# Performance work log

Hardware: AMD Instinct MI355X
Metric: run time of the kernel (lower is better)

Reference implementation:

```python
import jax, jax.numpy as jnp
import numpy as np

B, T, D, H = 2, 2048, 768, 12
HS = D // H           # head_size = 64
FF = 4 * D            # feed_forward_multiplier = 4 -> hidden 3072
HALF = FF // 2        # SwiGLU halves hidden -> 1536
EPS = 1e-8


def rmsnorm(x, scale):
    # RMSNorm with p=-1: full-dim L2 norm / sqrt(d), then x/(rms+eps)*scale
    d = x.shape[-1]
    rms = jnp.linalg.norm(x, axis=-1, keepdims=True) * (d ** -0.5)
    return scale * (x / (rms + EPS))


def setup_inputs() -> dict:
    key = jax.random.key(0)
    ks = jax.random.split(key, 12)
    s = 0.02
    return {
        "x":  jax.random.normal(ks[0], (B, T, D), dtype=jnp.float32),
        "Wq": jax.random.normal(ks[1], (H, D, HS), dtype=jnp.float32) * s,
        "Wk": jax.random.normal(ks[2], (H, D, HS), dtype=jnp.float32) * s,
        "Wv": jax.random.normal(ks[3], (H, D, HS), dtype=jnp.float32) * s,
        "Wo": jax.random.normal(ks[4], (D, D), dtype=jnp.float32) * s,
        "bo": jnp.zeros((D,), dtype=jnp.float32),
        "W1": jax.random.normal(ks[5], (D, FF), dtype=jnp.float32) * s,
        "b1": jnp.zeros((FF,), dtype=jnp.float32),
        "W2": jax.random.normal(ks[6], (HALF, D), dtype=jnp.float32) * s,
        "b2": jnp.zeros((D,), dtype=jnp.float32),
        "g1": jnp.ones((D,), dtype=jnp.float32),
        "g2": jnp.ones((D,), dtype=jnp.float32),
    }


def reference(x, Wq, Wk, Wv, Wo, bo, W1, b1, W2, b2, g1, g2):
    Bx, Tx, Dx = x.shape
    # --- Multi-head causal attention (pre-RMSNorm, residual) ---
    h = rmsnorm(x, g1)
    q = jnp.einsum('btd,hdk->bhtk', h, Wq)
    k = jnp.einsum('btd,hdk->bhtk', h, Wk)
    v = jnp.einsum('btd,hdk->bhtk', h, Wv)
    # NOTE: original scales by C**-0.5 where C = embed_dim (not head_size)
    scores = jnp.einsum('bhtk,bhsk->bhts', q, k) * (Dx ** -0.5)
    causal = jnp.tril(jnp.ones((Tx, Tx), dtype=bool))
    scores = jnp.where(causal, scores, -jnp.inf)
    wei = jax.nn.softmax(scores, axis=-1)
    attn = jnp.einsum('bhts,bhsk->bhtk', wei, v)
    attn = attn.transpose(0, 2, 1, 3).reshape(Bx, Tx, Dx)  # concat heads
    x = x + attn @ Wo + bo
    # --- SwiGLU FFN (pre-RMSNorm, residual) ---
    h2 = rmsnorm(x, g2)
    u = h2 @ W1 + b1
    a, gate = jnp.split(u, 2, axis=-1)  # chunk: first half = value, second = gate
    x = x + (jax.nn.silu(gate) * a) @ W2 + b2
    return x
```

## Files before the change

kernel.cpp:

```cpp
#include <hip/hip_runtime.h>
#include <math.h>

#define TDIM 2048
#define DDIM 768
#define NH   12
#define NROWS 4096
#define EPSV 1e-8f
#define SCALE 0.03608439182435161f

typedef __bf16 bf16_t;
typedef bf16_t bf16x8 __attribute__((ext_vector_type(8)));
typedef bf16_t bf16x4 __attribute__((ext_vector_type(4)));
typedef bf16_t bf16x2 __attribute__((ext_vector_type(2)));
typedef float  floatx4 __attribute__((ext_vector_type(4)));

__device__ __forceinline__ void glds16(const bf16_t* g, bf16_t* l) {
    __builtin_amdgcn_global_load_lds(
        (const __attribute__((address_space(1))) void*)g,
        (__attribute__((address_space(3))) void*)l, 16, 0, 0);
}

__global__ __launch_bounds__(256) void pack_rms(
    const float* __restrict__ Wq, const float* __restrict__ Wk,
    const float* __restrict__ Wv, const float* __restrict__ Wo,
    const float* __restrict__ W1, const float* __restrict__ W2,
    bf16_t* __restrict__ qkvw, bf16_t* __restrict__ wo,
    bf16_t* __restrict__ w1, bf16_t* __restrict__ w2,
    const float* __restrict__ x, const float* __restrict__ g1,
    bf16_t* __restrict__ hout)
{
    __shared__ float Ts[64][65];
    __shared__ float red[4];
    __shared__ float tot;
    int bid = blockIdx.x;
    int tid = threadIdx.x;

    if (bid >= 1440) {
        int row = bid - 1440;
        const float* xr = x + (size_t)row * DDIM;
        float v0 = xr[tid], v1 = xr[tid + 256], v2 = xr[tid + 512];
        float s = v0*v0 + v1*v1 + v2*v2;
        #pragma unroll
        for (int off = 32; off > 0; off >>= 1)
            s += __shfl_down(s, off, 64);
        if ((tid & 63) == 0) red[tid >> 6] = s;
        __syncthreads();
        if (tid == 0) tot = red[0] + red[1] + red[2] + red[3];
        __syncthreads();
        float rms = sqrtf(tot * (1.0f / DDIM));
        float inv = 1.0f / (rms + EPSV);
        bf16_t* orow = hout + (size_t)row * DDIM;
        orow[tid]       = (bf16_t)(g1[tid]       * v0 * inv);
        orow[tid + 256] = (bf16_t)(g1[tid + 256] * v1 * inv);
        orow[tid + 512] = (bf16_t)(g1[tid + 512] * v2 * inv);
        return;
    }

    const float* src; bf16_t* dst;
    int srcld, dstld, k0, n0;
    int remap = 0;
    if (bid < 144) {
        int kx = bid % 12, nx = bid / 12;
        src = Wo; dst = wo; srcld = 768; dstld = 768; k0 = kx * 64; n0 = nx * 64;
    } else if (bid < 720) {
        int t = bid - 144; int kx = t % 12, nx = t / 12;
        src = W1; dst = w1; srcld = 3072; dstld = 768; k0 = kx * 64; n0 = nx * 64;
        remap = 1;
    } else if (bid < 1008) {
        int t = bid - 720; int kx = t % 24, nx = t / 24;
        src = W2; dst = w2; srcld = 768; dstld = 1536; k0 = kx * 64; n0 = nx * 64;
    } else {
        int t = bid - 1008; int kx = t % 12, y = t / 12;
        int sel = y / 12, h = y - sel * 12;
        src = ((sel == 0) ? Wq : (sel == 1) ? Wk : Wv) + (size_t)h * 768 * 64;
        dst = qkvw + (size_t)(sel * 768 + h * 64) * 768;
        srcld = 64; dstld = 768; k0 = kx * 64; n0 = 0;
    }
    int r = tid >> 2, c = (tid & 3) * 16;
    const float* s = src + (size_t)(k0 + r) * srcld + n0 + c;
    #pragma unroll
    for (int i = 0; i < 4; i++) {
        float4 t = *(const float4*)(s + i * 4);
        Ts[r][c + i*4 + 0] = t.x; Ts[r][c + i*4 + 1] = t.y;
        Ts[r][c + i*4 + 2] = t.z; Ts[r][c + i*4 + 3] = t.w;
    }
    __syncthreads();
    int n = tid >> 2, kk = (tid & 3) * 16;
    bf16x8 o0, o1;
    #pragma unroll
    for (int i = 0; i < 8; i++) {
        o0[i] = (bf16_t)Ts[kk + i][n];
        o1[i] = (bf16_t)Ts[kk + 8 + i][n];
    }
    int oc = n0 + n;
    if (remap) oc = (oc < 1536) ? (oc * 2) : ((oc - 1536) * 2 + 1);
    bf16_t* d = dst + (size_t)oc * dstld + k0 + kk;
    *(bf16x8*)d = o0;
    *(bf16x8*)(d + 8) = o1;
}

__global__ __launch_bounds__(256) void rmsnorm_bf(
    const float* __restrict__ x, const float* __restrict__ g,
    bf16_t* __restrict__ out)
{
    int row = blockIdx.x;
    int tid = threadIdx.x;
    const float* xr = x + (size_t)row * DDIM;
    float v0 = xr[tid], v1 = xr[tid + 256], v2 = xr[tid + 512];
    float s = v0*v0 + v1*v1 + v2*v2;
    #pragma unroll
    for (int off = 32; off > 0; off >>= 1)
        s += __shfl_down(s, off, 64);
    __shared__ float red[4];
    __shared__ float tot;
    if ((tid & 63) == 0) red[tid >> 6] = s;
    __syncthreads();
    if (tid == 0) tot = red[0] + red[1] + red[2] + red[3];
    __syncthreads();
    float rms = sqrtf(tot * (1.0f / DDIM));
    float inv = 1.0f / (rms + EPSV);
    bf16_t* orow = out + (size_t)row * DDIM;
    orow[tid]       = (bf16_t)(g[tid]       * v0 * inv);
    orow[tid + 256] = (bf16_t)(g[tid + 256] * v1 * inv);
    orow[tid + 512] = (bf16_t)(g[tid + 512] * v2 * inv);
}

template<int TM, int EPI>
__global__ __launch_bounds__(256) void gemm_bf16(
    const bf16_t* __restrict__ A, const bf16_t* __restrict__ BT, int K,
    float* __restrict__ Cf, bf16_t* __restrict__ Cb, int ldc,
    const float* __restrict__ bias, const float* __restrict__ resid, int gx)
{
    constexpr int MT = TM / 32;
    __shared__ bf16_t As0[TM][32], As1[TM][32];
    __shared__ bf16_t Bs0[128][32], Bs1[128][32];
    int tid = threadIdx.x;
    int wave = tid >> 6, lane = tid & 63;
    int lrow = lane & 15, quad = lane >> 4;
    int wm = wave >> 1, wn = wave & 1;

    int flat = blockIdx.x;
    int cpx = gridDim.x >> 3;
    int swz = (flat & 7) * cpx + (flat >> 3);
    int m0 = (swz / gx) * TM;
    int n0 = (swz % gx) * 128;

    int srow = lane >> 2, scol = (lane & 3) * 8;
    const bf16_t* Ag = A  + ((size_t)m0 + wave * (TM/4) + srow) * K + scol;
    const bf16_t* Bg = BT + ((size_t)n0 + wave * 32 + srow) * K + scol;

    floatx4 acc[MT][4];
    #pragma unroll
    for (int mt = 0; mt < MT; mt++)
        #pragma unroll
        for (int nt = 0; nt < 4; nt++)
            #pragma unroll
            for (int r = 0; r < 4; r++) acc[mt][nt][r] = 0.f;

    for (int k0 = 0; k0 < K; k0 += 64) {
        __syncthreads();
        #pragma unroll
        for (int i = 0; i < TM/64; i++) {
            glds16(Ag + (size_t)(i*16) * K + k0,      &As0[wave*(TM/4) + i*16][0]);
            glds16(Ag + (size_t)(i*16) * K + k0 + 32, &As1[wave*(TM/4) + i*16][0]);
        }
        #pragma unroll
        for (int i = 0; i < 2; i++) {
            glds16(Bg + (size_t)(i*16) * K + k0,      &Bs0[wave*32 + i*16][0]);
            glds16(Bg + (size_t)(i*16) * K + k0 + 32, &Bs1[wave*32 + i*16][0]);
        }
        __syncthreads();

        bf16x8 af0[MT], af1[MT], bf0[4], bf1[4];
        #pragma unroll
        for (int mt = 0; mt < MT; mt++) {
            af0[mt] = *(const bf16x8*)&As0[wm*(TM/2) + mt*16 + lrow][quad * 8];
            af1[mt] = *(const bf16x8*)&As1[wm*(TM/2) + mt*16 + lrow][quad * 8];
        }
        #pragma unroll
        for (int nt = 0; nt < 4; nt++) {
            bf0[nt] = *(const bf16x8*)&Bs0[wn*64 + nt*16 + lrow][quad * 8];
            bf1[nt] = *(const bf16x8*)&Bs1[wn*64 + nt*16 + lrow][quad * 8];
        }
        #pragma unroll
        for (int mt = 0; mt < MT; mt++)
            #pragma unroll
            for (int nt = 0; nt < 4; nt++) {
                acc[mt][nt] = __builtin_amdgcn_mfma_f32_16x16x32_bf16(
                    bf0[nt], af0[mt], acc[mt][nt], 0, 0, 0);
                acc[mt][nt] = __builtin_amdgcn_mfma_f32_16x16x32_bf16(
                    bf1[nt], af1[mt], acc[mt][nt], 0, 0, 0);
            }
    }

    int crow0 = m0 + wm * (TM/2);
    int ccol0 = n0 + wn * 64;
    #pragma unroll
    for (int mt = 0; mt < MT; mt++) {
        int row = crow0 + mt * 16 + lrow;
        #pragma unroll
        for (int nt = 0; nt < 4; nt++) {
            int col = ccol0 + nt * 16 + quad * 4;
            floatx4 a = acc[mt][nt];
            if constexpr (EPI == 1) {
                int c = col >> 1;
                float2 ba = *(const float2*)(bias + c);
                float2 bg = *(const float2*)(bias + 1536 + c);
                float a0 = a[0] + ba.x, g0 = a[1] + bg.x;
                float a1 = a[2] + ba.y, g1 = a[3] + bg.y;
                bf16x2 v;
                v[0] = (bf16_t)(a0 * (g0 / (1.0f + __expf(-g0))));
                v[1] = (bf16_t)(a1 * (g1 / (1.0f + __expf(-g1))));
                *(bf16x2*)(Cb + (size_t)row * ldc + c) = v;
            } else {
                size_t off = (size_t)row * ldc + col;
                float4 bv = make_float4(0.f, 0.f, 0.f, 0.f);
                if (bias) bv = *(const float4*)(bias + col);
                float4 rs = make_float4(0.f, 0.f, 0.f, 0.f);
                if (resid) rs = *(const float4*)(resid + off);
                if (Cf) {
                    float4 v;
                    v.x = a[0] + bv.x + rs.x; v.y = a[1] + bv.y + rs.y;
                    v.z = a[2] + bv.z + rs.z; v.w = a[3] + bv.w + rs.w;
                    *(float4*)(Cf + off) = v;
                } else {
                    bf16x4 v;
                    v[0] = (bf16_t)(a[0] + bv.x + rs.x);
                    v[1] = (bf16_t)(a[1] + bv.y + rs.y);
                    v[2] = (bf16_t)(a[2] + bv.z + rs.z);
                    v[3] = (bf16_t)(a[3] + bv.w + rs.w);
                    *(bf16x4*)(Cb + off) = v;
                }
            }
        }
    }
}

__global__ __launch_bounds__(256) void vt_kernel(
    const bf16_t* __restrict__ qkv, bf16_t* __restrict__ vt)
{
    __shared__ bf16_t Ts[64][72];
    int t0 = blockIdx.x * 64;
    int bh = blockIdx.y;
    int b = bh / NH, h = bh - b * NH;
    int tid = threadIdx.x;
    int r = tid >> 2, c = (tid & 3) * 16;
    const bf16_t* src = qkv + ((size_t)b * TDIM + t0 + r) * 2304 + 1536 + h * 64 + c;
    *(bf16x8*)&Ts[r][c]     = *(const bf16x8*)src;
    *(bf16x8*)&Ts[r][c + 8] = *(const bf16x8*)(src + 8);
    __syncthreads();
    int d = tid >> 2, tt = (tid & 3) * 16;
    bf16x8 o0, o1;
    #pragma unroll
    for (int i = 0; i < 8; i++) {
        o0[i] = Ts[tt + i][d];
        o1[i] = Ts[tt + 8 + i][d];
    }
    bf16_t* dst = vt + ((size_t)bh * 64 + d) * TDIM + t0 + tt;
    *(bf16x8*)dst = o0;
    *(bf16x8*)(dst + 8) = o1;
}

__global__ __launch_bounds__(256) void attn_mfma(
    const bf16_t* __restrict__ qkv, const bf16_t* __restrict__ vt,
    bf16_t* __restrict__ o)
{
    const int QS = 2304;
    int bid = blockIdx.x;
    int c = bid & 255, slot = bid >> 8;
    int x = c & 31, g = c >> 5;
    int qt, bh;
    if (slot == 0)      { bh = g;      qt = x; }
    else if (slot == 1) { bh = 8 + g;  qt = (x + 16) & 31; }
    else                { bh = 16 + g; qt = (x < 16) ? (31 - 2 * x) : (62 - 2 * x); }
    int b = bh / NH, h = bh - b * NH;
    int tid = threadIdx.x;
    int wave = tid >> 6, lane = tid & 63;
    int lrow = lane & 15, quad = lane >> 4;

    __shared__ bf16_t Ks[2][64][72];
    __shared__ bf16_t Vts[2][64][72];
    __shared__ bf16_t Ps[4][16][72];

    size_t rbase = (size_t)b * TDIM;
    int q0 = qt * 64, qrow_w = q0 + wave * 16;

    const bf16_t* qp = qkv + (rbase + qrow_w + lrow) * QS + h * 64;
    bf16x8 qf[2];
    qf[0] = *(const bf16x8*)(qp + quad * 8);
    qf[1] = *(const bf16x8*)(qp + 32 + quad * 8);

    floatx4 o_acc[4];
    #pragma unroll
    for (int mt = 0; mt < 4; mt++)
        #pragma unroll
        for (int r = 0; r < 4; r++) o_acc[mt][r] = 0.f;
    float m_r = -INFINITY, l_r = 0.f;

    int srow = tid >> 2;
    int scol = (tid & 3) * 16;
    const bf16_t* kbase = qkv + (rbase + srow) * QS + 768 + h * 64 + scol;
    const bf16_t* vbase = vt + ((size_t)bh * 64 + srow) * TDIM + scol;

    bf16x8 kr0 = *(const bf16x8*)kbase;
    bf16x8 kr1 = *(const bf16x8*)(kbase + 8);
    bf16x8 vr0 = *(const bf16x8*)vbase;
    bf16x8 vr1 = *(const bf16x8*)(vbase + 8);
    *(bf16x8*)&Ks[0][srow][scol]      = kr0;
    *(bf16x8*)&Ks[0][srow][scol + 8]  = kr1;
    *(bf16x8*)&Vts[0][srow][scol]     = vr0;
    *(bf16x8*)&Vts[0][srow][scol + 8] = vr1;
    if (qt >= 1) {
        const bf16_t* kp = kbase + (size_t)64 * QS;
        const bf16_t* vp = vbase + 64;
        kr0 = *(const bf16x8*)kp;  kr1 = *(const bf16x8*)(kp + 8);
        vr0 = *(const bf16x8*)vp;  vr1 = *(const bf16x8*)(vp + 8);
    }
    asm volatile("s_waitcnt lgkmcnt(0)" ::: "memory");
    __builtin_amdgcn_s_barrier();

    for (int s = 0; s <= qt; s++) {
        int cur = s & 1;

        floatx4 sfrag[4];
        __builtin_amdgcn_s_setprio(1);
        #pragma unroll
        for (int nt = 0; nt < 4; nt++) {
            floatx4 a;
            #pragma unroll
            for (int r = 0; r < 4; r++) a[r] = 0.f;
            #pragma unroll
            for (int kf = 0; kf < 2; kf++) {
                bf16x8 afr = *(const bf16x8*)&Ks[cur][nt * 16 + lrow][kf * 32 + quad * 8];
                a = __builtin_amdgcn_mfma_f32_16x16x32_bf16(afr, qf[kf], a, 0, 0, 0);
            }
            sfrag[nt] = a;
        }
        __builtin_amdgcn_s_setprio(0);

        if (s < qt) {
            int nxt = cur ^ 1;
            *(bf16x8*)&Ks[nxt][srow][scol]      = kr0;
            *(bf16x8*)&Ks[nxt][srow][scol + 8]  = kr1;
            *(bf16x8*)&Vts[nxt][srow][scol]     = vr0;
            *(bf16x8*)&Vts[nxt][srow][scol + 8] = vr1;
        }

        if (s == qt) {
            int qg = qrow_w + lrow;
            #pragma unroll
            for (int nt = 0; nt < 4; nt++)
                #pragma unroll
                for (int r = 0; r < 4; r++) {
                    int kc = s * 64 + nt * 16 + quad * 4 + r;
                    sfrag[nt][r] = (kc > qg) ? -INFINITY : sfrag[nt][r] * SCALE;
                }
        } else {
            #pragma unroll
            for (int nt = 0; nt < 4; nt++)
                #pragma unroll
                for (int r = 0; r < 4; r++) sfrag[nt][r] *= SCALE;
        }

        float mx = sfrag[0][0];
        #pragma unroll
        for (int nt = 0; nt < 4; nt++)
            #pragma unroll
            for (int r = 0; r < 4; r++) mx = fmaxf(mx, sfrag[nt][r]);
        mx = fmaxf(mx, __shfl_xor(mx, 16, 64));
        mx = fmaxf(mx, __shfl_xor(mx, 32, 64));
        if (__any(mx > m_r + 8.0f)) {
            float mn = fmaxf(m_r, mx);
            float alpha = __expf(m_r - mn);
            m_r = mn;
            l_r *= alpha;
            #pragma unroll
            for (int mt = 0; mt < 4; mt++)
                #pragma unroll
                for (int r = 0; r < 4; r++) o_acc[mt][r] *= alpha;
        }

        float ls = 0.f;
        #pragma unroll
        for (int nt = 0; nt < 4; nt++) {
            bf16x4 pv;
            #pragma unroll
            for (int r = 0; r < 4; r++) {
                float p = __expf(sfrag[nt][r] - m_r);
                ls += p;
                pv[r] = (bf16_t)p;
            }
            *(bf16x4*)&Ps[wave][lrow][nt * 16 + quad * 4] = pv;
        }
        ls += __shfl_xor(ls, 16, 64);
        ls += __shfl_xor(ls, 32, 64);
        l_r += ls;

        __builtin_amdgcn_s_setprio(1);
        #pragma unroll
        for (int kf = 0; kf < 2; kf++) {
            bf16x8 pfr = *(const bf16x8*)&Ps[wave][lrow][kf * 32 + quad * 8];
            #pragma unroll
            for (int mt = 0; mt < 4; mt++) {
                bf16x8 vfr = *(const bf16x8*)&Vts[cur][mt * 16 + lrow][kf * 32 + quad * 8];
                o_acc[mt] = __builtin_amdgcn_mfma_f32_16x16x32_bf16(vfr, pfr, o_acc[mt], 0, 0, 0);
            }
        }
        __builtin_amdgcn_s_setprio(0);

        if (s + 2 <= qt) {
            const bf16_t* kp = kbase + (size_t)(s + 2) * 64 * QS;
            const bf16_t* vp = vbase + (size_t)(s + 2) * 64;
            kr0 = *(const bf16x8*)kp;  kr1 = *(const bf16x8*)(kp + 8);
            vr0 = *(const bf16x8*)vp;  vr1 = *(const bf16x8*)(vp + 8);
        }

        asm volatile("s_waitcnt lgkmcnt(0)" ::: "memory");
        __builtin_amdgcn_s_barrier();
    }

    float inv = 1.0f / l_r;
    size_t rb = (rbase + qrow_w + lrow) * DDIM + h * 64;
    #pragma unroll
    for (int mt = 0; mt < 4; mt++) {
        bf16x4 ov;
        #pragma unroll
        for (int r = 0; r < 4; r++) ov[r] = (bf16_t)(o_acc[mt][r] * inv);
        *(bf16x4*)(o + rb + mt * 16 + quad * 4) = ov;
    }
}

extern "C" void kernel_launch(void* const* d_in, const int* in_sizes, int n_in,
                              void* d_out, int out_size, void* d_ws, size_t ws_size,
                              hipStream_t stream) {
    const float* x  = (const float*)d_in[0];
    const float* Wq = (const float*)d_in[1];
    const float* Wk = (const float*)d_in[2];
    const float* Wv = (const float*)d_in[3];
    const float* Wo = (const float*)d_in[4];
    const float* bo = (const float*)d_in[5];
    const float* W1 = (const float*)d_in[6];
    const float* b1 = (const float*)d_in[7];
    const float* W2 = (const float*)d_in[8];
    const float* b2 = (const float*)d_in[9];
    const float* g1 = (const float*)d_in[10];
    const float* g2 = (const float*)d_in[11];
    float* out = (float*)d_out;
    char* ws = (char*)d_ws;

    bf16_t* qkvw_bt = (bf16_t*)(ws);
    bf16_t* wo_bt   = (bf16_t*)(ws + 3538944);
    bf16_t* w1_bt   = (bf16_t*)(ws + 4718592);
    bf16_t* w2_bt   = (bf16_t*)(ws + 9437184);
    bf16_t* h_bf    = (bf16_t*)(ws + 11796480);
    bf16_t* qkv     = (bf16_t*)(ws + 18087936);
    bf16_t* attn_bf = (bf16_t*)(ws + 36962304);
    bf16_t* sw_bf   = (bf16_t*)(ws + 68419584);
    bf16_t* vt      = (bf16_t*)(ws + 81002496);

    pack_rms<<<5536, 256, 0, stream>>>(Wq, Wk, Wv, Wo, W1, W2,
                                       qkvw_bt, wo_bt, w1_bt, w2_bt,
                                       x, g1, h_bf);

    gemm_bf16<128, 0><<<576, 256, 0, stream>>>(
        h_bf, qkvw_bt, 768, nullptr, qkv, 2304, nullptr, nullptr, 18);

    vt_kernel<<<dim3(32, 24), 256, 0, stream>>>(qkv, vt);

    attn_mfma<<<768, 256, 0, stream>>>(qkv, vt, attn_bf);

    gemm_bf16<64, 0><<<384, 256, 0, stream>>>(
        attn_bf, wo_bt, 768, out, nullptr, 768, bo, x, 6);

    rmsnorm_bf<<<NROWS, 256, 0, stream>>>(out, g2, h_bf);

    gemm_bf16<128, 1><<<768, 256, 0, stream>>>(
        h_bf, w1_bt, 768, nullptr, sw_bf, 1536, b1, nullptr, 24);

    gemm_bf16<64, 0><<<384, 256, 0, stream>>>(
        sw_bf, w2_bt, 1536, out, nullptr, 768, b2, out, 6);
}
```

Baseline: 260.2 us.

## Rewrite attention with 32x32 MFMA, 128-row query tiles and register-resident P

The attention kernel now uses 32x32x16 bf16 MFMA with each wave owning 32 query rows, so a block covers 128 query rows and the grid halves to 384 blocks. The P tile stays in registers and is rearranged with cross-half lane shuffles into the B-operand layout, which removes the LDS round trip for P. A new block-to-tile mapping pairs heavy and light causal tiles for load balance, and waves whose rows are fully masked skip compute on the extra K tile. The cost is more registers per wave and fewer blocks available to fill the GPU.

```diff
diff --git a/kernel.cpp b/kernel.cpp
--- a/kernel.cpp
+++ b/kernel.cpp
@@ -13,6 +13,7 @@
 typedef bf16_t bf16x4 __attribute__((ext_vector_type(4)));
 typedef bf16_t bf16x2 __attribute__((ext_vector_type(2)));
 typedef float  floatx4 __attribute__((ext_vector_type(4)));
+typedef float  f32x16 __attribute__((ext_vector_type(16)));
 
 __device__ __forceinline__ void glds16(const bf16_t* g, bf16_t* l) {
     __builtin_amdgcn_global_load_lds(
@@ -267,34 +268,35 @@
 {
     const int QS = 2304;
     int bid = blockIdx.x;
-    int c = bid & 255, slot = bid >> 8;
-    int x = c & 31, g = c >> 5;
-    int qt, bh;
-    if (slot == 0)      { bh = g;      qt = x; }
-    else if (slot == 1) { bh = 8 + g;  qt = (x + 16) & 31; }
-    else                { bh = 16 + g; qt = (x < 16) ? (31 - 2 * x) : (62 - 2 * x); }
+    int idx;
+    if (bid >= 128 && bid < 256) idx = 168 + (bid - 128);
+    else if (bid < 128)          idx = bid;
+    else { int p = 511 - bid; idx = (p >= 168) ? p + 128 : p; }
+    int t = idx / 24, bh = idx % 24;
     int b = bh / NH, h = bh - b * NH;
     int tid = threadIdx.x;
     int wave = tid >> 6, lane = tid & 63;
-    int lrow = lane & 15, quad = lane >> 4;
+    int l31 = lane & 31, hi = lane >> 5;
 
     __shared__ bf16_t Ks[2][64][72];
     __shared__ bf16_t Vts[2][64][72];
-    __shared__ bf16_t Ps[4][16][72];
 
     size_t rbase = (size_t)b * TDIM;
-    int q0 = qt * 64, qrow_w = q0 + wave * 16;
-
-    const bf16_t* qp = qkv + (rbase + qrow_w + lrow) * QS + h * 64;
-    bf16x8 qf[2];
-    qf[0] = *(const bf16x8*)(qp + quad * 8);
-    qf[1] = *(const bf16x8*)(qp + 32 + quad * 8);
-
-    floatx4 o_acc[4];
-    #pragma unroll
-    for (int mt = 0; mt < 4; mt++)
-        #pragma unroll
-        for (int r = 0; r < 4; r++) o_acc[mt][r] = 0.f;
+    int st = 2 * t + 1;
+    int qtw = st - 1 + (wave >> 1);
+    int q0w = t * 128 + wave * 32;
+
+    const bf16_t* qp = qkv + (rbase + q0w + l31) * QS + h * 64;
+    bf16x8 qf[4];
+    #pragma unroll
+    for (int ds = 0; ds < 4; ds++)
+        qf[ds] = *(const bf16x8*)(qp + ds * 16 + hi * 8);
+
+    f32x16 o_acc[2];
+    #pragma unroll
+    for (int dt = 0; dt < 2; dt++)
+        #pragma unroll
+        for (int r = 0; r < 16; r++) o_acc[dt][r] = 0.f;
     float m_r = -INFINITY, l_r = 0.f;
 
     int srow = tid >> 2;
@@ -310,7 +312,7 @@
     *(bf16x8*)&Ks[0][srow][scol + 8]  = kr1;
     *(bf16x8*)&Vts[0][srow][scol]     = vr0;
     *(bf16x8*)&Vts[0][srow][scol + 8] = vr1;
-    if (qt >= 1) {
+    {
         const bf16_t* kp = kbase + (size_t)64 * QS;
         const bf16_t* vp = vbase + 64;
         kr0 = *(const bf16x8*)kp;  kr1 = *(const bf16x8*)(kp + 8);
@@ -319,26 +321,30 @@
     asm volatile("s_waitcnt lgkmcnt(0)" ::: "memory");
     __builtin_amdgcn_s_barrier();
 
-    for (int s = 0; s <= qt; s++) {
+    for (int s = 0; s <= st; s++) {
         int cur = s & 1;
-
-        floatx4 sfrag[4];
-        __builtin_amdgcn_s_setprio(1);
-        #pragma unroll
-        for (int nt = 0; nt < 4; nt++) {
-            floatx4 a;
-            #pragma unroll
-            for (int r = 0; r < 4; r++) a[r] = 0.f;
-            #pragma unroll
-            for (int kf = 0; kf < 2; kf++) {
-                bf16x8 afr = *(const bf16x8*)&Ks[cur][nt * 16 + lrow][kf * 32 + quad * 8];
-                a = __builtin_amdgcn_mfma_f32_16x16x32_bf16(afr, qf[kf], a, 0, 0, 0);
+        int live = (s <= qtw);
+
+        f32x16 sf[2];
+        if (live) {
+            #pragma unroll
+            for (int kct = 0; kct < 2; kct++) {
+                #pragma unroll
+                for (int r = 0; r < 16; r++) sf[kct][r] = 0.f;
             }
-            sfrag[nt] = a;
-        }
-        __builtin_amdgcn_s_setprio(0);
-
-        if (s < qt) {
+            __builtin_amdgcn_s_setprio(1);
+            #pragma unroll
+            for (int kct = 0; kct < 2; kct++)
+                #pragma unroll
+                for (int ds = 0; ds < 4; ds++) {
+                    bf16x8 afr = *(const bf16x8*)&Ks[cur][kct*32 + l31][ds*16 + hi*8];
+                    sf[kct] = __builtin_amdgcn_mfma_f32_32x32x16_bf16(
+                        afr, qf[ds], sf[kct], 0, 0, 0);
+                }
+            __builtin_amdgcn_s_setprio(0);
+        }
+
+        if (s < st) {
             int nxt = cur ^ 1;
             *(bf16x8*)&Ks[nxt][srow][scol]      = kr0;
             *(bf16x8*)&Ks[nxt][srow][scol + 8]  = kr1;
@@ -346,69 +352,84 @@
             *(bf16x8*)&Vts[nxt][srow][scol + 8] = vr1;
         }
 
-        if (s == qt) {
-            int qg = qrow_w + lrow;
-            #pragma unroll
-            for (int nt = 0; nt < 4; nt++)
-                #pragma unroll
-                for (int r = 0; r < 4; r++) {
-                    int kc = s * 64 + nt * 16 + quad * 4 + r;
-                    sfrag[nt][r] = (kc > qg) ? -INFINITY : sfrag[nt][r] * SCALE;
+        if (live) {
+            if (s == qtw) {
+                int qg = q0w + l31;
+                #pragma unroll
+                for (int kct = 0; kct < 2; kct++)
+                    #pragma unroll
+                    for (int r = 0; r < 16; r++) {
+                        int kc = s*64 + kct*32 + (r&3) + 8*(r>>2) + 4*hi;
+                        sf[kct][r] = (kc > qg) ? -INFINITY : sf[kct][r] * SCALE;
+                    }
+            } else {
+                #pragma unroll
+                for (int kct = 0; kct < 2; kct++)
+                    #pragma unroll
+                    for (int r = 0; r < 16; r++) sf[kct][r] *= SCALE;
+            }
+
+            float mx = sf[0][0];
+            #pragma unroll
+            for (int kct = 0; kct < 2; kct++)
+                #pragma unroll
+                for (int r = 0; r < 16; r++) mx = fmaxf(mx, sf[kct][r]);
+            mx = fmaxf(mx, __shfl_xor(mx, 32, 64));
+            if (__any(mx > m_r + 8.0f)) {
+                float mn = fmaxf(m_r, mx);
+                float alpha = __expf(m_r - mn);
+                m_r = mn;
+                l_r *= alpha;
+                #pragma unroll
+                for (int dt = 0; dt < 2; dt++)
+                    #pragma unroll
+                    for (int r = 0; r < 16; r++) o_acc[dt][r] *= alpha;
+            }
+            float ls = 0.f;
+            #pragma unroll
+            for (int kct = 0; kct < 2; kct++)
+                #pragma unroll
+                for (int r = 0; r < 16; r++) {
+                    float e = __expf(sf[kct][r] - m_r);
+                    ls += e;
+                    sf[kct][r] = e;
                 }
-        } else {
-            #pragma unroll
-            for (int nt = 0; nt < 4; nt++)
-                #pragma unroll
-                for (int r = 0; r < 4; r++) sfrag[nt][r] *= SCALE;
-        }
-
-        float mx = sfrag[0][0];
-        #pragma unroll
-        for (int nt = 0; nt < 4; nt++)
-            #pragma unroll
-            for (int r = 0; r < 4; r++) mx = fmaxf(mx, sfrag[nt][r]);
-        mx = fmaxf(mx, __shfl_xor(mx, 16, 64));
-        mx = fmaxf(mx, __shfl_xor(mx, 32, 64));
-        if (__any(mx > m_r + 8.0f)) {
-            float mn = fmaxf(m_r, mx);
-            float alpha = __expf(m_r - mn);
-            m_r = mn;
-            l_r *= alpha;
-            #pragma unroll
-            for (int mt = 0; mt < 4; mt++)
-                #pragma unroll
-                for (int r = 0; r < 4; r++) o_acc[mt][r] *= alpha;
-        }
-
-        float ls = 0.f;
-        #pragma unroll
-        for (int nt = 0; nt < 4; nt++) {
-            bf16x4 pv;
-            #pragma unroll
-            for (int r = 0; r < 4; r++) {
-                float p = __expf(sfrag[nt][r] - m_r);
-                ls += p;
-                pv[r] = (bf16_t)p;
+            ls += __shfl_xor(ls, 32, 64);
+            l_r += ls;
+
+            __builtin_amdgcn_s_setprio(1);
+            #pragma unroll
+            for (int ks = 0; ks < 4; ks++) {
+                int kct = ks >> 1, base = (ks & 1) * 8;
+                bf16x4 A, Bv;
+                #pragma unroll
+                for (int j = 0; j < 4; j++) {
+                    A[j]  = (bf16_t)sf[kct][base + j];
+                    Bv[j] = (bf16_t)sf[kct][base + 4 + j];
+                }
+                int2 ai = *(int2*)&A, bi = *(int2*)&Bv;
+                int2 ra, rb2;
+                ra.x  = __shfl_xor(ai.x, 32, 64);
+                ra.y  = __shfl_xor(ai.y, 32, 64);
+                rb2.x = __shfl_xor(bi.x, 32, 64);
+                rb2.y = __shfl_xor(bi.y, 32, 64);
+                int4 pd;
+                pd.x = hi ? rb2.x : ai.x;
+                pd.y = hi ? rb2.y : ai.y;
+                pd.z = hi ? bi.x : ra.x;
+                pd.w = hi ? bi.y : ra.y;
+                bf16x8 pb = *(bf16x8*)&pd;
+                #pragma unroll
+                for (int dt = 0; dt < 2; dt++) {
+                    bf16x8 vfr = *(const bf16x8*)&Vts[cur][dt*32 + l31][ks*16 + hi*8];
+                    o_acc[dt] = __builtin_amdgcn_mfma_f32_32x32x16_bf16(
+                        vfr, pb, o_acc[dt], 0, 0, 0);
+                }
             }
-            *(bf16x4*)&Ps[wave][lrow][nt * 16 + quad * 4] = pv;
-        }
-        ls += __shfl_xor(ls, 16, 64);
-        ls += __shfl_xor(ls, 32, 64);
-        l_r += ls;
-
-        __builtin_amdgcn_s_setprio(1);
-        #pragma unroll
-        for (int kf = 0; kf < 2; kf++) {
-            bf16x8 pfr = *(const bf16x8*)&Ps[wave][lrow][kf * 32 + quad * 8];
-            #pragma unroll
-            for (int mt = 0; mt < 4; mt++) {
-                bf16x8 vfr = *(const bf16x8*)&Vts[cur][mt * 16 + lrow][kf * 32 + quad * 8];
-                o_acc[mt] = __builtin_amdgcn_mfma_f32_16x16x32_bf16(vfr, pfr, o_acc[mt], 0, 0, 0);
-            }
-        }
-        __builtin_amdgcn_s_setprio(0);
-
-        if (s + 2 <= qt) {
+            __builtin_amdgcn_s_setprio(0);
+        }
+
+        if (s + 2 <= st) {
             const bf16_t* kp = kbase + (size_t)(s + 2) * 64 * QS;
             const bf16_t* vp = vbase + (size_t)(s + 2) * 64;
             kr0 = *(const bf16x8*)kp;  kr1 = *(const bf16x8*)(kp + 8);
@@ -420,14 +441,17 @@
     }
 
     float inv = 1.0f / l_r;
-    size_t rb = (rbase + qrow_w + lrow) * DDIM + h * 64;
-    #pragma unroll
-    for (int mt = 0; mt < 4; mt++) {
-        bf16x4 ov;
-        #pragma unroll
-        for (int r = 0; r < 4; r++) ov[r] = (bf16_t)(o_acc[mt][r] * inv);
-        *(bf16x4*)(o + rb + mt * 16 + quad * 4) = ov;
-    }
+    size_t rb = (rbase + q0w + l31) * DDIM + h * 64;
+    #pragma unroll
+    for (int dt = 0; dt < 2; dt++)
+        #pragma unroll
+        for (int J = 0; J < 4; J++) {
+            bf16x4 ov;
+            #pragma unroll
+            for (int rr = 0; rr < 4; rr++)
+                ov[rr] = (bf16_t)(o_acc[dt][4*J + rr] * inv);
+            *(bf16x4*)(o + rb + dt*32 + 8*J + 4*hi) = ov;
+        }
 }
 
 extern "C" void kernel_launch(void* const* d_in, const int* in_sizes, int n_in,
@@ -467,7 +491,7 @@
 
     vt_kernel<<<dim3(32, 24), 256, 0, stream>>>(qkv, vt);
 
-    attn_mfma<<<768, 256, 0, stream>>>(qkv, vt, attn_bf);
+    attn_mfma<<<384, 256, 0, stream>>>(qkv, vt, attn_bf);
 
     gemm_bf16<64, 0><<<384, 256, 0, stream>>>(
         attn_bf, wo_bt, 768, out, nullptr, 768, bo, x, 6);
```

Measured after the change: 272.0 us. 1.05x slower.
